# Performance work log

Measured on AMD Instinct MI355X. Metric: run time of the kernel, lower is better.

## Reference

```python
import jax, jax.numpy as jnp
import numpy as np

GATE_THRESH = 0.4
LN_EPS = 1e-5
NORM_EPS = 1e-12  # torch F.normalize eps


def setup_inputs() -> dict:
    key = jax.random.key(0)
    ks = jax.random.split(key, 8)
    B, L, H, V = 64, 1024, 64, 32000
    s = lambda k, shape, scale: (jax.random.normal(k, shape, jnp.float32) * scale)
    return {
        "seq": jax.random.randint(ks[0], (B, L), 0, V),
        "embed": s(ks[1], (V, H), 0.02),
        "W1": s(ks[2], (H, 2 * H), 0.05), "b1": jnp.zeros((2 * H,), jnp.float32),
        "W2": s(ks[3], (2 * H, H), 0.05), "b2": jnp.zeros((H,), jnp.float32),
        "gamma": jnp.ones((H,), jnp.float32), "beta": jnp.zeros((H,), jnp.float32),
        "kpW": s(ks[4], (H, H), 0.1),
        "rpW": s(ks[5], (H, H), 0.1), "rpb": jnp.zeros((H,), jnp.float32),
        "outW": s(ks[6], (H, V), 0.05), "outb": jnp.zeros((V,), jnp.float32),
    }


def reference(seq, embed, W1, b1, W2, b2, gamma, beta, kpW, rpW, rpb, outW, outb):
    # embed + FF residual + LayerNorm
    h = embed[seq]                                        # (B,L,H)
    ffo = jax.nn.relu(h @ W1 + b1) @ W2 + b2
    x = h + ffo
    mu = x.mean(-1, keepdims=True)
    var = x.var(-1, keepdims=True)                        # biased, like torch LN
    h = (x - mu) * jax.lax.rsqrt(var + LN_EPS) * gamma + beta

    k_all = h @ kpW                                       # kp projection for all t, (B,L,H)
    B, L, H = h.shape

    def step(M, k):                                       # M: (B,H,H), k: (B,H)
        kn = k / jnp.maximum(jnp.linalg.norm(k, axis=-1, keepdims=True), NORM_EPS)
        vp = jnp.einsum('bij,bj->bi', M, kn)
        err = k - vp
        gate = (jnp.linalg.norm(err, axis=-1) >= GATE_THRESH * jnp.linalg.norm(k, axis=-1)).astype(k.dtype)
        Delta = gate[:, None, None] * err[:, :, None] * kn[:, None, :]
        return M + Delta, None                            # use_ema=False -> plain accumulation

    M0 = jnp.zeros((B, H, H), h.dtype)
    M, _ = jax.lax.scan(step, M0, jnp.swapaxes(k_all[:, :-1], 0, 1))  # scan over L-1 steps

    q = k_all[:, -1]                                      # query from last token
    read = jnp.einsum('bij,bj->bi', M, q)
    return (read @ rpW + rpb) @ outW + outb               # (B,V)
```

## Files before the change

kernel.cpp:

```cpp
#include <hip/hip_runtime.h>
#include <hip/hip_bf16.h>

#define HDIM 64
#define LSEQ 1024
#define NB 64
#define NV 32000
#define CC 32
#define NCH 32
#define NT (NB * LSEQ)

template<int CTRL>
__device__ __forceinline__ float dpp_red(float x) {
  int y = __builtin_amdgcn_update_dpp(0, __float_as_int(x), CTRL, 0xF, 0xF, true);
  return x + __int_as_float(y);
}
__device__ __forceinline__ float quad_sum(float x) {
  x = dpp_red<0xB1>(x);
  x = dpp_red<0x4E>(x);
  return x;
}
__device__ __forceinline__ float wave_sum(float x) {
  x = dpp_red<0xB1>(x);
  x = dpp_red<0x4E>(x);
  x = dpp_red<0x141>(x);
  x = dpp_red<0x140>(x);
  float a = __int_as_float(__builtin_amdgcn_readlane(__float_as_int(x), 0));
  float b = __int_as_float(__builtin_amdgcn_readlane(__float_as_int(x), 16));
  float c = __int_as_float(__builtin_amdgcn_readlane(__float_as_int(x), 32));
  float d = __int_as_float(__builtin_amdgcn_readlane(__float_as_int(x), 48));
  return (a + b) + (c + d);
}

__global__ __launch_bounds__(256) void transpose_w(const float* __restrict__ W1,
    const float* __restrict__ kpW, float* __restrict__ W1T, float* __restrict__ kpWT)
{
  const int tid = blockIdx.x * 256 + threadIdx.x;
  if (tid < 8192) { const int c = tid >> 6, j = tid & 63; W1T[tid] = W1[j * 128 + c]; }
  else { const int e = tid - 8192; const int i = e >> 6, j = e & 63; kpWT[e] = kpW[j * 64 + i]; }
}

__global__ __launch_bounds__(256, 1) void tok4(
    const int* __restrict__ seq, const float* __restrict__ embed,
    const float* __restrict__ W1T, const float* __restrict__ b1,
    const float* __restrict__ W2, const float* __restrict__ b2,
    const float* __restrict__ gamma, const float* __restrict__ beta,
    const float* __restrict__ kpWT, float* __restrict__ kallT,
    float* __restrict__ thr2_all, float* __restrict__ inv_all)
{
  const int tok = blockIdx.x * 256 + threadIdx.x;
  const int row = seq[tok];
  float h[64], x[64];
  const float4* ep = (const float4*)(embed + (size_t)row * HDIM);
  #pragma unroll
  for (int q = 0; q < 16; ++q) {
    const float4 v = ep[q];
    h[4*q] = v.x; h[4*q+1] = v.y; h[4*q+2] = v.z; h[4*q+3] = v.w;
  }
  #pragma unroll
  for (int j = 0; j < 64; ++j) x[j] = h[j] + b2[j];

  for (int c = 0; c < 128; ++c) {
    const float* w1r = W1T + c * 64;
    float a0 = 0.f, a1 = 0.f, a2 = 0.f, a3 = 0.f;
    #pragma unroll
    for (int j = 0; j < 64; j += 4) {
      a0 = fmaf(h[j],   w1r[j],   a0);
      a1 = fmaf(h[j+1], w1r[j+1], a1);
      a2 = fmaf(h[j+2], w1r[j+2], a2);
      a3 = fmaf(h[j+3], w1r[j+3], a3);
    }
    const float y = fmaxf(b1[c] + ((a0 + a1) + (a2 + a3)), 0.f);
    const float* w2r = W2 + c * 64;
    #pragma unroll
    for (int j = 0; j < 64; ++j) x[j] = fmaf(y, w2r[j], x[j]);
  }

  float s0=0.f,s1=0.f,s2=0.f,s3=0.f,q0=0.f,q1=0.f,q2=0.f,q3=0.f;
  #pragma unroll
  for (int j = 0; j < 64; j += 4) {
    s0 += x[j]; s1 += x[j+1]; s2 += x[j+2]; s3 += x[j+3];
    q0 = fmaf(x[j],   x[j],   q0); q1 = fmaf(x[j+1], x[j+1], q1);
    q2 = fmaf(x[j+2], x[j+2], q2); q3 = fmaf(x[j+3], x[j+3], q3);
  }
  const float mu  = ((s0+s1)+(s2+s3)) * (1.f/64.f);
  const float var = ((q0+q1)+(q2+q3)) * (1.f/64.f) - mu * mu;
  const float rs  = rsqrtf(var + 1e-5f);
  #pragma unroll
  for (int j = 0; j < 64; ++j) h[j] = (x[j] - mu) * rs * gamma[j] + beta[j];

  float nk2 = 0.f;
  for (int i = 0; i < 64; ++i) {
    const float* kr = kpWT + i * 64;
    float c0=0.f,c1=0.f,c2=0.f,c3=0.f;
    #pragma unroll
    for (int j = 0; j < 64; j += 4) {
      c0 = fmaf(h[j],   kr[j],   c0);
      c1 = fmaf(h[j+1], kr[j+1], c1);
      c2 = fmaf(h[j+2], kr[j+2], c2);
      c3 = fmaf(h[j+3], kr[j+3], c3);
    }
    const float ki = (c0 + c1) + (c2 + c3);
    nk2 = fmaf(ki, ki, nk2);
    kallT[(size_t)i * NT + tok] = ki;
  }
  thr2_all[tok] = 0.16f * nk2;
  inv_all[tok]  = 1.f / fmaxf(sqrtf(nk2), 1e-12f);
}

__global__ __launch_bounds__(64) void gram2(const float* __restrict__ kallT,
    const float* __restrict__ inv_all, float* __restrict__ Gg)
{
  const int bi = blockIdx.x;
  const int b = bi >> 5, ch = bi & 31;
  const int l = threadIdx.x;
  const int t0 = (l & 7) * 4, s0 = (l >> 3) * 4;
  const size_t gb = (size_t)b * LSEQ + ch * CC;
  float g00=0,g01=0,g02=0,g03=0, g10=0,g11=0,g12=0,g13=0;
  float g20=0,g21=0,g22=0,g23=0, g30=0,g31=0,g32=0,g33=0;
  for (int j = 0; j < 64; ++j) {
    const float* rowp = kallT + (size_t)j * NT + gb;
    const float4 a = *(const float4*)(rowp + t0);
    const float4 c = *(const float4*)(rowp + s0);
    g00=fmaf(a.x,c.x,g00); g01=fmaf(a.x,c.y,g01); g02=fmaf(a.x,c.z,g02); g03=fmaf(a.x,c.w,g03);
    g10=fmaf(a.y,c.x,g10); g11=fmaf(a.y,c.y,g11); g12=fmaf(a.y,c.z,g12); g13=fmaf(a.y,c.w,g13);
    g20=fmaf(a.z,c.x,g20); g21=fmaf(a.z,c.y,g21); g22=fmaf(a.z,c.z,g22); g23=fmaf(a.z,c.w,g23);
    g30=fmaf(a.w,c.x,g30); g31=fmaf(a.w,c.y,g31); g32=fmaf(a.w,c.z,g32); g33=fmaf(a.w,c.w,g33);
  }
  const float4 it = *(const float4*)(inv_all + gb + t0);
  const float4 is = *(const float4*)(inv_all + gb + s0);
  float* Go = Gg + (size_t)bi * (CC * CC);
  float4 o;
  o.x=g00*it.x*is.x; o.y=g01*it.x*is.y; o.z=g02*it.x*is.z; o.w=g03*it.x*is.w;
  *(float4*)(Go + (t0+0)*CC + s0) = o;
  o.x=g10*it.y*is.x; o.y=g11*it.y*is.y; o.z=g12*it.y*is.z; o.w=g13*it.y*is.w;
  *(float4*)(Go + (t0+1)*CC + s0) = o;
  o.x=g20*it.z*is.x; o.y=g21*it.z*is.y; o.z=g22*it.z*is.z; o.w=g23*it.z*is.w;
  *(float4*)(Go + (t0+2)*CC + s0) = o;
  o.x=g30*it.w*is.x; o.y=g31*it.w*is.y; o.z=g32*it.w*is.z; o.w=g33*it.w*is.w;
  *(float4*)(Go + (t0+3)*CC + s0) = o;
}

__global__ __launch_bounds__(192, 1) void scan6(
    const float* __restrict__ kallT, const float* __restrict__ thr2_all,
    const float* __restrict__ inv_all, const float* __restrict__ Gg,
    float* __restrict__ readv)
{
  __shared__ float kS[3][CC * 68];
  __shared__ float GS[2][CC * CC];
  __shared__ float rS[CC * 64];
  __shared__ float cstS[CC * 64];
  __shared__ float thr2S[2][CC];
  __shared__ float invS[3][CC];

  const int b = blockIdx.x, tid = threadIdx.x;
  const int w = tid >> 6, l = tid & 63;
  const int A = l >> 2, B4 = l & 3;
  const int r0 = 32 * (w - 1) + 2 * A;
  const int jb = 16 * B4;
  const size_t gbase = (size_t)b * LSEQ;

  float M0[16], M1[16], acc[32];
  #pragma unroll
  for (int q = 0; q < 16; ++q) { M0[q] = 0.f; M1[q] = 0.f; }

#define A2_SLICE(KB, IB, T0) do {                                              \
    _Pragma("unroll")                                                          \
    for (int t = (T0); t < (T0) + 8; ++t) {                                    \
      const float* kr = &kS[KB][t * 68 + jb];                                  \
      float p0a=0.f,p0b=0.f,p1a=0.f,p1b=0.f;                                   \
      _Pragma("unroll")                                                        \
      for (int q2 = 0; q2 < 4; ++q2) {                                         \
        const float4 kv = ((const float4*)kr)[q2];                             \
        p0a = fmaf(M0[4*q2+0], kv.x, p0a); p0b = fmaf(M0[4*q2+1], kv.y, p0b);  \
        p0a = fmaf(M0[4*q2+2], kv.z, p0a); p0b = fmaf(M0[4*q2+3], kv.w, p0b);  \
        p1a = fmaf(M1[4*q2+0], kv.x, p1a); p1b = fmaf(M1[4*q2+1], kv.y, p1b);  \
        p1a = fmaf(M1[4*q2+2], kv.z, p1a); p1b = fmaf(M1[4*q2+3], kv.w, p1b);  \
      }                                                                        \
      float p0 = quad_sum(p0a + p0b);                                          \
      float p1 = quad_sum(p1a + p1b);                                          \
      const float iv = invS[IB][t];                                            \
      if (B4 == 0) *(float2*)&rS[t * 64 + r0] = make_float2(p0 * iv, p1 * iv); \
    }                                                                          \
  } while (0)

#define C_SLICE(KB, IB, S0) do {                                               \
    _Pragma("unroll")                                                          \
    for (int s = (S0); s < (S0) + 8; ++s) {                                    \
      const float2 cc2 = *(const float2*)&cstS[s * 64 + r0];                   \
      const float iv = invS[IB][s];                                            \
      const float c0 = cc2.x * iv, c1 = cc2.y * iv;                            \
      const float* kr = &kS[KB][s * 68 + jb];                                  \
      _Pragma("unroll")                                                        \
      for (int q2 = 0; q2 < 4; ++q2) {                                         \
        const float4 kv = ((const float4*)kr)[q2];                             \
        M0[4*q2+0] = fmaf(c0, kv.x, M0[4*q2+0]); M0[4*q2+1] = fmaf(c0, kv.y, M0[4*q2+1]); \
        M0[4*q2+2] = fmaf(c0, kv.z, M0[4*q2+2]); M0[4*q2+3] = fmaf(c0, kv.w, M0[4*q2+3]); \
        M1[4*q2+0] = fmaf(c1, kv.x, M1[4*q2+0]); M1[4*q2+1] = fmaf(c1, kv.y, M1[4*q2+1]); \
        M1[4*q2+2] = fmaf(c1, kv.z, M1[4*q2+2]); M1[4*q2+3] = fmaf(c1, kv.w, M1[4*q2+3]); \
      }                                                                        \
    }                                                                          \
  } while (0)

#define B_SLICE(Q, CBUF, CGI, LASTCH) do {                                     \
    const int t0_ = 8 * (Q);                                                   \
    _Pragma("unroll")                                                          \
    for (int i = 0; i < 8; ++i) {                                              \
      const int u = t0_ + i;                                                   \
      acc[u] += kS[CBUF][u * 68 + l] - rS[u * 64 + l];                         \
    }                                                                          \
    const float4 tha = ((const float4*)&thr2S[CGI][t0_])[0];                   \
    const float4 thb = ((const float4*)&thr2S[CGI][t0_])[1];                   \
    const float th8[8] = {tha.x,tha.y,tha.z,tha.w, thb.x,thb.y,thb.z,thb.w};   \
    _Pragma("unroll")                                                          \
    for (int i = 0; i < 8; ++i) {                                              \
      const int t = t0_ + i;                                                   \
      float g[32];                                                             \
      const float4* gp = (const float4*)&GS[CGI][t * 32];                      \
      _Pragma("unroll")                                                        \
      for (int r = 0; r < 8; ++r) {                                            \
        const float4 v = gp[r];                                                \
        g[4*r]=v.x; g[4*r+1]=v.y; g[4*r+2]=v.z; g[4*r+3]=v.w;                  \
      }                                                                        \
      const float err = acc[t];                                                \
      const float ne2 = wave_sum(err * err);                                   \
      bool gate = (ne2 >= th8[i]);                                             \
      if ((LASTCH) && t == CC - 1) gate = false;                               \
      const float c = gate ? err : 0.f;                                        \
      cstS[t * 64 + l] = c;                                                    \
      _Pragma("unroll")                                                        \
      for (int u = 0; u < 32; ++u) acc[u] = fmaf(-g[u], c, acc[u]);            \
    }                                                                          \
  } while (0)

  if (w < 2) {
    const float* src = kallT + (size_t)l * NT + gbase + w * 16;
    #pragma unroll
    for (int q = 0; q < 4; ++q) {
      const float4 v = ((const float4*)src)[q];
      const int t0 = w * 16 + q * 4;
      kS[0][(t0+0)*68 + l] = v.x; kS[0][(t0+1)*68 + l] = v.y;
      kS[0][(t0+2)*68 + l] = v.z; kS[0][(t0+3)*68 + l] = v.w;
    }
  } else {
    const float4* gsrc = (const float4*)(Gg + (size_t)b * NCH * (CC * CC));
    #pragma unroll
    for (int q = 0; q < 4; ++q) ((float4*)GS[0])[q * 64 + l] = gsrc[q * 64 + l];
    if (l < CC) thr2S[0][l] = thr2_all[gbase + l];
    else        invS[0][l - CC] = inv_all[gbase + (l - CC)];
  }
  __syncthreads();

  for (int ch = 0; ch < NCH; ++ch) {
    const int cb = ch % 3, pb = (ch + 2) % 3, nb = (ch + 1) % 3;
    const int cg = ch & 1, ng = 1 - cg;
    const bool lastch = (ch == NCH - 1);

    if (w == 0) {
      #pragma unroll
      for (int u = 0; u < 32; ++u) acc[u] = 0.f;
      if (!lastch) {
        const float* src = kallT + (size_t)l * NT + gbase + (ch + 1) * CC;
        #pragma unroll
        for (int q = 0; q < 8; ++q) {
          const float4 v = ((const float4*)src)[q];
          const int t0 = q * 4;
          kS[nb][(t0+0)*68 + l] = v.x; kS[nb][(t0+1)*68 + l] = v.y;
          kS[nb][(t0+2)*68 + l] = v.z; kS[nb][(t0+3)*68 + l] = v.w;
        }
        const float4* gsrc = (const float4*)(Gg + ((size_t)b * NCH + ch + 1) * (CC * CC));
        #pragma unroll
        for (int q = 0; q < 4; ++q) ((float4*)GS[ng])[q * 64 + l] = gsrc[q * 64 + l];
        if (l < CC) thr2S[ng][l] = thr2_all[gbase + (ch + 1) * CC + l];
        else        invS[nb][l - CC] = inv_all[gbase + (ch + 1) * CC + (l - CC)];
      }
    } else {
      if (ch > 0) C_SLICE(pb, pb, 24);
      A2_SLICE(cb, cb, 0);
    }
    __syncthreads();

    if (w == 0) B_SLICE(0, cb, cg, lastch);
    else        A2_SLICE(cb, cb, 8);
    __syncthreads();
    if (w == 0) B_SLICE(1, cb, cg, lastch);
    else        A2_SLICE(cb, cb, 16);
    __syncthreads();
    if (w == 0) B_SLICE(2, cb, cg, lastch);
    else { A2_SLICE(cb, cb, 24); C_SLICE(cb, cb, 0); }
    __syncthreads();
    if (w == 0) B_SLICE(3, cb, cg, lastch);
    else { C_SLICE(cb, cb, 8); C_SLICE(cb, cb, 16); }
    __syncthreads();
  }

  {
    constexpr int fb = (NCH - 1) % 3;
    if (w > 0) {
      C_SLICE(fb, fb, 24);
      const float* kr = &kS[fb][(CC - 1) * 68 + jb];
      float p0a=0.f,p0b=0.f,p1a=0.f,p1b=0.f;
      #pragma unroll
      for (int q2 = 0; q2 < 4; ++q2) {
        const float4 kv = ((const float4*)kr)[q2];
        p0a = fmaf(M0[4*q2+0], kv.x, p0a); p0b = fmaf(M0[4*q2+1], kv.y, p0b);
        p0a = fmaf(M0[4*q2+2], kv.z, p0a); p0b = fmaf(M0[4*q2+3], kv.w, p0b);
        p1a = fmaf(M1[4*q2+0], kv.x, p1a); p1b = fmaf(M1[4*q2+1], kv.y, p1b);
        p1a = fmaf(M1[4*q2+2], kv.z, p1a); p1b = fmaf(M1[4*q2+3], kv.w, p1b);
      }
      float d0 = quad_sum(p0a + p0b);
      float d1 = quad_sum(p1a + p1b);
      if (B4 == 0) *(float2*)&readv[b * 64 + r0] = make_float2(d0, d1);
    }
  }
#undef A2_SLICE
#undef C_SLICE
#undef B_SLICE
}

__global__ __launch_bounds__(64) void rproj_kernel(const float* __restrict__ readv,
    const float* __restrict__ rpW, const float* __restrict__ rpb, float* __restrict__ r2T)
{
  const int b = blockIdx.x, i = threadIdx.x;
  const float* rv = readv + b * 64;
  float acc = rpb[i];
  #pragma unroll
  for (int j = 0; j < 64; ++j)
    acc = fmaf(rv[j], rpW[j * 64 + i], acc);
  r2T[i * 64 + b] = acc;
}

__global__ __launch_bounds__(256, 1) void out_kernel(const float* __restrict__ r2T,
    const float* __restrict__ outW, const float* __restrict__ outb,
    float* __restrict__ out)
{
  const int v = blockIdx.x * 256 + threadIdx.x;
  float acc[64];
  #pragma unroll
  for (int b = 0; b < 64; ++b) acc[b] = 0.f;
  for (int k = 0; k < 64; ++k) {
    const float wv = outW[(size_t)k * NV + v];
    const float* rr = r2T + k * 64;
    #pragma unroll
    for (int b = 0; b < 64; ++b)
      acc[b] = fmaf(rr[b], wv, acc[b]);
  }
  const float ob = outb[v];
  #pragma unroll
  for (int b = 0; b < 64; ++b)
    out[(size_t)b * NV + v] = acc[b] + ob;
}

extern "C" void kernel_launch(void* const* d_in, const int* in_sizes, int n_in,
                              void* d_out, int out_size, void* d_ws, size_t ws_size,
                              hipStream_t stream)
{
  const int*   seq   = (const int*)d_in[0];
  const float* embed = (const float*)d_in[1];
  const float* W1    = (const float*)d_in[2];
  const float* b1    = (const float*)d_in[3];
  const float* W2    = (const float*)d_in[4];
  const float* b2    = (const float*)d_in[5];
  const float* gam   = (const float*)d_in[6];
  const float* bet   = (const float*)d_in[7];
  const float* kpW   = (const float*)d_in[8];
  const float* rpW   = (const float*)d_in[9];
  const float* rpb   = (const float*)d_in[10];
  const float* outW  = (const float*)d_in[11];
  const float* outb  = (const float*)d_in[12];
  float* out = (float*)d_out;

  float* ws = (float*)d_ws;
  float* kallT = ws;
  float* G     = kallT + (size_t)HDIM * NT;
  float* thr2  = G     + (size_t)NB * NCH * CC * CC;
  float* inv   = thr2  + NT;
  float* readv = inv   + NT;
  float* r2T   = readv + NB * HDIM;
  float* W1T   = r2T   + NB * HDIM;
  float* kpWT  = W1T   + 8192;

  hipLaunchKernelGGL(transpose_w, dim3(48), dim3(256), 0, stream, W1, kpW, W1T, kpWT);
  hipLaunchKernelGGL(tok4, dim3(256), dim3(256), 0, stream,
                     seq, embed, W1T, b1, W2, b2, gam, bet, kpWT, kallT, thr2, inv);
  hipLaunchKernelGGL(gram2, dim3(NB * NCH), dim3(64), 0, stream, kallT, inv, G);
  hipLaunchKernelGGL(scan6, dim3(NB), dim3(192), 0, stream, kallT, thr2, inv, G, readv);
  hipLaunchKernelGGL(rproj_kernel, dim3(NB), dim3(64), 0, stream, readv, rpW, rpb, r2T);
  hipLaunchKernelGGL(out_kernel, dim3(NV / 256), dim3(256), 0, stream, r2T, outW, outb, out);
}
```

Baseline: 483.7 us.

## Restructure chunked scan into two phases and stage gram tiles in LDS

The gram kernel now loads a 128-token slab of k into shared memory once per block and computes four 32x32 chunk Gram matrices from it, instead of one 64-thread block per chunk reading global memory. The scan kernel drops its shared-memory double buffers for G, thresholds and inverse norms and reads them straight from global memory. The per-chunk schedule shrinks from four barrier-separated stages of 8 tokens to two stages of 16. The residual k - Mk is now formed in the A phase, and the gate-update loop is triangular, touching only later tokens. Fewer barriers and less redundant FMA work per chunk come at the cost of global-load latency sitting on the serial wave-0 critical path.

```diff
diff --git a/kernel.cpp b/kernel.cpp
--- a/kernel.cpp
+++ b/kernel.cpp
@@ -107,18 +107,32 @@
   inv_all[tok]  = 1.f / fmaxf(sqrtf(nk2), 1e-12f);
 }
 
-__global__ __launch_bounds__(64) void gram2(const float* __restrict__ kallT,
+__global__ __launch_bounds__(256, 1) void gram3(const float* __restrict__ kallT,
     const float* __restrict__ inv_all, float* __restrict__ Gg)
 {
+  __shared__ float kS4[64 * 128];
   const int bi = blockIdx.x;
-  const int b = bi >> 5, ch = bi & 31;
-  const int l = threadIdx.x;
+  const int b = bi >> 3, g4 = bi & 7;
+  const int tid = threadIdx.x;
+  const size_t gb = (size_t)b * LSEQ + g4 * 128;
+
+  #pragma unroll
+  for (int q = 0; q < 8; ++q) {
+    const int e = q * 256 + tid;
+    const int j = e >> 5, p = e & 31;
+    ((float4*)kS4)[(j << 5) + p] =
+        *(const float4*)(kallT + (size_t)j * NT + gb + p * 4);
+  }
+  __syncthreads();
+
+  const int w = tid >> 6, l = tid & 63;
+  const int tb = w * 32;
   const int t0 = (l & 7) * 4, s0 = (l >> 3) * 4;
-  const size_t gb = (size_t)b * LSEQ + ch * CC;
   float g00=0,g01=0,g02=0,g03=0, g10=0,g11=0,g12=0,g13=0;
   float g20=0,g21=0,g22=0,g23=0, g30=0,g31=0,g32=0,g33=0;
+  #pragma unroll 8
   for (int j = 0; j < 64; ++j) {
-    const float* rowp = kallT + (size_t)j * NT + gb;
+    const float* rowp = kS4 + j * 128 + tb;
     const float4 a = *(const float4*)(rowp + t0);
     const float4 c = *(const float4*)(rowp + s0);
     g00=fmaf(a.x,c.x,g00); g01=fmaf(a.x,c.y,g01); g02=fmaf(a.x,c.z,g02); g03=fmaf(a.x,c.w,g03);
@@ -126,9 +140,9 @@
     g20=fmaf(a.z,c.x,g20); g21=fmaf(a.z,c.y,g21); g22=fmaf(a.z,c.z,g22); g23=fmaf(a.z,c.w,g23);
     g30=fmaf(a.w,c.x,g30); g31=fmaf(a.w,c.y,g31); g32=fmaf(a.w,c.z,g32); g33=fmaf(a.w,c.w,g33);
   }
-  const float4 it = *(const float4*)(inv_all + gb + t0);
-  const float4 is = *(const float4*)(inv_all + gb + s0);
-  float* Go = Gg + (size_t)bi * (CC * CC);
+  const float4 it = *(const float4*)(inv_all + gb + tb + t0);
+  const float4 is = *(const float4*)(inv_all + gb + tb + s0);
+  float* Go = Gg + ((size_t)b * NCH + g4 * 4 + w) * (CC * CC);
   float4 o;
   o.x=g00*it.x*is.x; o.y=g01*it.x*is.y; o.z=g02*it.x*is.z; o.w=g03*it.x*is.w;
   *(float4*)(Go + (t0+0)*CC + s0) = o;
@@ -140,17 +154,14 @@
   *(float4*)(Go + (t0+3)*CC + s0) = o;
 }
 
-__global__ __launch_bounds__(192, 1) void scan6(
+__global__ __launch_bounds__(192, 1) void scan7(
     const float* __restrict__ kallT, const float* __restrict__ thr2_all,
     const float* __restrict__ inv_all, const float* __restrict__ Gg,
     float* __restrict__ readv)
 {
   __shared__ float kS[3][CC * 68];
-  __shared__ float GS[2][CC * CC];
   __shared__ float rS[CC * 64];
   __shared__ float cstS[CC * 64];
-  __shared__ float thr2S[2][CC];
-  __shared__ float invS[3][CC];
 
   const int b = blockIdx.x, tid = threadIdx.x;
   const int w = tid >> 6, l = tid & 63;
@@ -163,9 +174,9 @@
   #pragma unroll
   for (int q = 0; q < 16; ++q) { M0[q] = 0.f; M1[q] = 0.f; }
 
-#define A2_SLICE(KB, IB, T0) do {                                              \
+#define A2_SLICE(KB, IVP, T0) do {                                             \
     _Pragma("unroll")                                                          \
-    for (int t = (T0); t < (T0) + 8; ++t) {                                    \
+    for (int t = (T0); t < (T0) + 16; ++t) {                                   \
       const float* kr = &kS[KB][t * 68 + jb];                                  \
       float p0a=0.f,p0b=0.f,p1a=0.f,p1b=0.f;                                   \
       _Pragma("unroll")                                                        \
@@ -178,16 +189,19 @@
       }                                                                        \
       float p0 = quad_sum(p0a + p0b);                                          \
       float p1 = quad_sum(p1a + p1b);                                          \
-      const float iv = invS[IB][t];                                            \
-      if (B4 == 0) *(float2*)&rS[t * 64 + r0] = make_float2(p0 * iv, p1 * iv); \
+      const float iv = (IVP)[t];                        \
+      const float2 kv2 = *(const float2*)&kS[KB][t * 68 + r0];                 \
+      if (B4 == 0)                                                             \
+        *(float2*)&rS[t * 64 + r0] = make_float2(kv2.x - p0 * iv,              \
+                                                 kv2.y - p1 * iv);             \
     }                                                                          \
   } while (0)
 
-#define C_SLICE(KB, IB, S0) do {                                               \
+#define C_SLICE(KB, IVP, S0) do {                                              \
     _Pragma("unroll")                                                          \
-    for (int s = (S0); s < (S0) + 8; ++s) {                                    \
+    for (int s = (S0); s < (S0) + 16; ++s) {                                   \
       const float2 cc2 = *(const float2*)&cstS[s * 64 + r0];                   \
-      const float iv = invS[IB][s];                                            \
+      const float iv = (IVP)[s];                        \
       const float c0 = cc2.x * iv, c1 = cc2.y * iv;                            \
       const float* kr = &kS[KB][s * 68 + jb];                                  \
       _Pragma("unroll")                                                        \
@@ -201,34 +215,22 @@
     }                                                                          \
   } while (0)
 
-#define B_SLICE(Q, CBUF, CGI, LASTCH) do {                                     \
-    const int t0_ = 8 * (Q);                                                   \
+#define B_SLICE(Q, GROW, THP, LASTCH) do {                                     \
+    const int t0_ = 16 * (Q);                                                  \
     _Pragma("unroll")                                                          \
-    for (int i = 0; i < 8; ++i) {                                              \
-      const int u = t0_ + i;                                                   \
-      acc[u] += kS[CBUF][u * 68 + l] - rS[u * 64 + l];                         \
-    }                                                                          \
-    const float4 tha = ((const float4*)&thr2S[CGI][t0_])[0];                   \
-    const float4 thb = ((const float4*)&thr2S[CGI][t0_])[1];                   \
-    const float th8[8] = {tha.x,tha.y,tha.z,tha.w, thb.x,thb.y,thb.z,thb.w};   \
+    for (int i = 0; i < 16; ++i) acc[t0_ + i] += rS[(t0_ + i) * 64 + l];       \
     _Pragma("unroll")                                                          \
-    for (int i = 0; i < 8; ++i) {                                              \
+    for (int i = 0; i < 16; ++i) {                                             \
       const int t = t0_ + i;                                                   \
-      float g[32];                                                             \
-      const float4* gp = (const float4*)&GS[CGI][t * 32];                      \
-      _Pragma("unroll")                                                        \
-      for (int r = 0; r < 8; ++r) {                                            \
-        const float4 v = gp[r];                                                \
-        g[4*r]=v.x; g[4*r+1]=v.y; g[4*r+2]=v.z; g[4*r+3]=v.w;                  \
-      }                                                                        \
+      const float* grow = (GROW) + t * CC;              \
       const float err = acc[t];                                                \
       const float ne2 = wave_sum(err * err);                                   \
-      bool gate = (ne2 >= th8[i]);                                             \
+      bool gate = (ne2 >= (THP)[t]);                                           \
       if ((LASTCH) && t == CC - 1) gate = false;                               \
       const float c = gate ? err : 0.f;                                        \
       cstS[t * 64 + l] = c;                                                    \
       _Pragma("unroll")                                                        \
-      for (int u = 0; u < 32; ++u) acc[u] = fmaf(-g[u], c, acc[u]);            \
+      for (int u = t + 1; u < CC; ++u) acc[u] = fmaf(-grow[u], c, acc[u]);     \
     }                                                                          \
   } while (0)
 
@@ -241,19 +243,16 @@
       kS[0][(t0+0)*68 + l] = v.x; kS[0][(t0+1)*68 + l] = v.y;
       kS[0][(t0+2)*68 + l] = v.z; kS[0][(t0+3)*68 + l] = v.w;
     }
-  } else {
-    const float4* gsrc = (const float4*)(Gg + (size_t)b * NCH * (CC * CC));
-    #pragma unroll
-    for (int q = 0; q < 4; ++q) ((float4*)GS[0])[q * 64 + l] = gsrc[q * 64 + l];
-    if (l < CC) thr2S[0][l] = thr2_all[gbase + l];
-    else        invS[0][l - CC] = inv_all[gbase + (l - CC)];
   }
   __syncthreads();
 
   for (int ch = 0; ch < NCH; ++ch) {
     const int cb = ch % 3, pb = (ch + 2) % 3, nb = (ch + 1) % 3;
-    const int cg = ch & 1, ng = 1 - cg;
     const bool lastch = (ch == NCH - 1);
+    const float* ivcur = inv_all  + gbase + ch * CC;
+    const float* ivprv = inv_all  + gbase + (ch - 1) * CC;
+    const float* thcur = thr2_all + gbase + ch * CC;
+    const float* Grow  = Gg + ((size_t)b * NCH + ch) * (CC * CC);
 
     if (w == 0) {
       #pragma unroll
@@ -267,50 +266,39 @@
           kS[nb][(t0+0)*68 + l] = v.x; kS[nb][(t0+1)*68 + l] = v.y;
           kS[nb][(t0+2)*68 + l] = v.z; kS[nb][(t0+3)*68 + l] = v.w;
         }
-        const float4* gsrc = (const float4*)(Gg + ((size_t)b * NCH + ch + 1) * (CC * CC));
-        #pragma unroll
-        for (int q = 0; q < 4; ++q) ((float4*)GS[ng])[q * 64 + l] = gsrc[q * 64 + l];
-        if (l < CC) thr2S[ng][l] = thr2_all[gbase + (ch + 1) * CC + l];
-        else        invS[nb][l - CC] = inv_all[gbase + (ch + 1) * CC + (l - CC)];
       }
     } else {
-      if (ch > 0) C_SLICE(pb, pb, 24);
-      A2_SLICE(cb, cb, 0);
+      if (ch > 0) C_SLICE(pb, ivprv, 16);
+      A2_SLICE(cb, ivcur, 0);
     }
     __syncthreads();
 
-    if (w == 0) B_SLICE(0, cb, cg, lastch);
-    else        A2_SLICE(cb, cb, 8);
+    if (w == 0) B_SLICE(0, Grow, thcur, lastch);
+    else        A2_SLICE(cb, ivcur, 16);
     __syncthreads();
-    if (w == 0) B_SLICE(1, cb, cg, lastch);
-    else        A2_SLICE(cb, cb, 16);
+
+    if (w == 0) B_SLICE(1, Grow, thcur, lastch);
+    else        C_SLICE(cb, ivcur, 0);
     __syncthreads();
-    if (w == 0) B_SLICE(2, cb, cg, lastch);
-    else { A2_SLICE(cb, cb, 24); C_SLICE(cb, cb, 0); }
-    __syncthreads();
-    if (w == 0) B_SLICE(3, cb, cg, lastch);
-    else { C_SLICE(cb, cb, 8); C_SLICE(cb, cb, 16); }
-    __syncthreads();
-  }
-
-  {
+  }
+
+  if (w > 0) {
     constexpr int fb = (NCH - 1) % 3;
-    if (w > 0) {
-      C_SLICE(fb, fb, 24);
-      const float* kr = &kS[fb][(CC - 1) * 68 + jb];
-      float p0a=0.f,p0b=0.f,p1a=0.f,p1b=0.f;
-      #pragma unroll
-      for (int q2 = 0; q2 < 4; ++q2) {
-        const float4 kv = ((const float4*)kr)[q2];
-        p0a = fmaf(M0[4*q2+0], kv.x, p0a); p0b = fmaf(M0[4*q2+1], kv.y, p0b);
-        p0a = fmaf(M0[4*q2+2], kv.z, p0a); p0b = fmaf(M0[4*q2+3], kv.w, p0b);
-        p1a = fmaf(M1[4*q2+0], kv.x, p1a); p1b = fmaf(M1[4*q2+1], kv.y, p1b);
-        p1a = fmaf(M1[4*q2+2], kv.z, p1a); p1b = fmaf(M1[4*q2+3], kv.w, p1b);
-      }
-      float d0 = quad_sum(p0a + p0b);
-      float d1 = quad_sum(p1a + p1b);
-      if (B4 == 0) *(float2*)&readv[b * 64 + r0] = make_float2(d0, d1);
-    }
+    const float* iv31 = inv_all + gbase + (NCH - 1) * CC;
+    C_SLICE(fb, iv31, 16);
+    const float* kr = &kS[fb][(CC - 1) * 68 + jb];
+    float p0a=0.f,p0b=0.f,p1a=0.f,p1b=0.f;
+    #pragma unroll
+    for (int q2 = 0; q2 < 4; ++q2) {
+      const float4 kv = ((const float4*)kr)[q2];
+      p0a = fmaf(M0[4*q2+0], kv.x, p0a); p0b = fmaf(M0[4*q2+1], kv.y, p0b);
+      p0a = fmaf(M0[4*q2+2], kv.z, p0a); p0b = fmaf(M0[4*q2+3], kv.w, p0b);
+      p1a = fmaf(M1[4*q2+0], kv.x, p1a); p1b = fmaf(M1[4*q2+1], kv.y, p1b);
+      p1a = fmaf(M1[4*q2+2], kv.z, p1a); p1b = fmaf(M1[4*q2+3], kv.w, p1b);
+    }
+    float d0 = quad_sum(p0a + p0b);
+    float d1 = quad_sum(p1a + p1b);
+    if (B4 == 0) *(float2*)&readv[b * 64 + r0] = make_float2(d0, d1);
   }
 #undef A2_SLICE
 #undef C_SLICE
@@ -382,8 +370,8 @@
   hipLaunchKernelGGL(transpose_w, dim3(48), dim3(256), 0, stream, W1, kpW, W1T, kpWT);
   hipLaunchKernelGGL(tok4, dim3(256), dim3(256), 0, stream,
                      seq, embed, W1T, b1, W2, b2, gam, bet, kpWT, kallT, thr2, inv);
-  hipLaunchKernelGGL(gram2, dim3(NB * NCH), dim3(64), 0, stream, kallT, inv, G);
-  hipLaunchKernelGGL(scan6, dim3(NB), dim3(192), 0, stream, kallT, thr2, inv, G, readv);
+  hipLaunchKernelGGL(gram3, dim3(NB * 8), dim3(256), 0, stream, kallT, inv, G);
+  hipLaunchKernelGGL(scan7, dim3(NB), dim3(192), 0, stream, kallT, thr2, inv, G, readv);
   hipLaunchKernelGGL(rproj_kernel, dim3(NB), dim3(64), 0, stream, readv, rpW, rpb, r2T);
   hipLaunchKernelGGL(out_kernel, dim3(NV / 256), dim3(256), 0, stream, r2T, outW, outb, out);
 }
```

New measurement: 624.9 us. +29.2%, slower.
